# Performance work log

Hardware: AMD Instinct MI355X
Metric: run time of the kernel (lower is better)

The kernel has to match this reference:

```python
import jax, jax.numpy as jnp
import numpy as np

NUM_NODES = 100000
EMBED_DIM = 64
NUM_LAYERS = 3
NUM_EDGES = 1250000


def setup_inputs() -> dict:
    key = jax.random.key(0)
    k1, k2 = jax.random.split(key)
    edge_index = jax.random.randint(k1, (2, NUM_EDGES), 0, NUM_NODES, dtype=jnp.int64)
    emb_weight = jax.random.normal(k2, (NUM_NODES, EMBED_DIM), dtype=jnp.float32)
    alpha = jnp.full((NUM_LAYERS + 1,), 1.0 / (NUM_LAYERS + 1), dtype=jnp.float32)
    return {"edge_index": edge_index, "emb_weight": emb_weight, "alpha": alpha}


def reference(edge_index, emb_weight, alpha):
    # edge_index: [2, E] int; emb_weight: [N, d]; alpha: [L+1]
    row, col = edge_index[0], edge_index[1]  # source, target (flow source_to_target)
    N = emb_weight.shape[0]

    # gcn_norm without self-loops: deg over target index, symmetric normalization
    deg = jax.ops.segment_sum(jnp.ones_like(row, dtype=emb_weight.dtype), col, num_segments=N)
    dis = jnp.where(deg > 0, jax.lax.rsqrt(jnp.maximum(deg, 1.0)), 0.0)
    w = dis[row] * dis[col]  # [E]

    x = emb_weight
    out = x * alpha[0]
    for i in range(NUM_LAYERS):
        # gather-scale-scatter: out[col] += w * x[row]
        msg = x[row] * w[:, None]  # [E, d]
        x = jax.ops.segment_sum(msg, col, num_segments=N)
        out = out + x * alpha[i + 1]

    # edge_label_index defaults to edge_index -> dot-product ranking per edge
    return jnp.sum(out[row] * out[col], axis=-1)  # [E]
```

## Files before the change

### kernel.cpp

```cpp
#include <hip/hip_runtime.h>

#define EDIM 64
#define CHUNK 4096
#define BSH 9
#define BCOLS 512
#define CAP 8192
#define PAD 8
#define MAXPADB ((PAD - 1) * BCOLS)

__device__ __forceinline__ unsigned f2_to_bf2(float a, float b) {
    unsigned ua = __float_as_uint(a); ua += 0x7fffu + ((ua >> 16) & 1u);
    unsigned ub = __float_as_uint(b); ub += 0x7fffu + ((ub >> 16) & 1u);
    return (ua >> 16) | (ub & 0xffff0000u);
}
__device__ __forceinline__ float bf_lo(unsigned u) { return __uint_as_float(u << 16); }
__device__ __forceinline__ float bf_hi(unsigned u) { return __uint_as_float(u & 0xffff0000u); }

__global__ void k_binit(int* __restrict__ bcur, int nb) {
    int b = threadIdx.x;
    if (b < nb) bcur[b] = b * CAP;
}

__global__ __launch_bounds__(256) void k_binA(const int* __restrict__ row, const int* __restrict__ col,
                                              int* __restrict__ bcur, uint2* __restrict__ pairs,
                                              int E, int nb) {
    __shared__ uint2 buf[CHUNK];
    __shared__ int histL[256], baseL[256], curL[256], gbaseL[256];
    __shared__ int wsum[4];
    int tid = threadIdx.x;
    int c0 = blockIdx.x * CHUNK;
    int cend = min(CHUNK, E - c0);

    histL[tid] = 0;
    __syncthreads();

    int myr[CHUNK / 256], myc[CHUNK / 256];
    #pragma unroll
    for (int k = 0; k < CHUNK / 256; ++k) {
        int i = k * 256 + tid;
        if (i < cend) {
            int e = c0 + i;
            myr[k] = row[e]; myc[k] = col[e];
            atomicAdd(&histL[myc[k] >> BSH], 1);
        }
    }
    __syncthreads();

    int v = histL[tid];
    int lane = tid & 63, w = tid >> 6;
    int inc = v;
    #pragma unroll
    for (int d = 1; d < 64; d <<= 1) { int t = __shfl_up(inc, d, 64); if (lane >= d) inc += t; }
    if (lane == 63) wsum[w] = inc;
    __syncthreads();
    int woff = 0;
    for (int i = 0; i < w; ++i) woff += wsum[i];
    int excl = inc - v + woff;
    baseL[tid] = excl;
    curL[tid] = excl;
    if (tid < nb) gbaseL[tid] = atomicAdd(&bcur[tid], v);
    __syncthreads();

    #pragma unroll
    for (int k = 0; k < CHUNK / 256; ++k) {
        int i = k * 256 + tid;
        if (i < cend) {
            int b = myc[k] >> BSH;
            int e = c0 + i;
            int pos = atomicAdd(&curL[b], 1);
            buf[pos] = make_uint2((unsigned)myr[k] | ((unsigned)b << 24),
                                  ((unsigned)e << 9) | ((unsigned)myc[k] & (BCOLS - 1)));
        }
    }
    __syncthreads();

    for (int i = tid; i < cend; i += 256) {
        uint2 p = buf[i];
        int b = (int)(p.x >> 24);
        int dst = gbaseL[b] + (i - baseL[b]);
        pairs[dst] = make_uint2(p.x & 0x00FFFFFFu, p.y);
    }
}

__global__ void k_bscan(const int* __restrict__ bcur, int* __restrict__ bbase, int nb) {
    __shared__ int wsum[4];
    int tid = threadIdx.x;
    int v = (tid < nb) ? (bcur[tid] - tid * CAP) : 0;
    int lane = tid & 63, w = tid >> 6;
    int inc = v;
    #pragma unroll
    for (int d = 1; d < 64; d <<= 1) { int t = __shfl_up(inc, d, 64); if (lane >= d) inc += t; }
    if (lane == 63) wsum[w] = inc;
    __syncthreads();
    int woff = 0;
    for (int i = 0; i < w; ++i) woff += wsum[i];
    if (tid < nb) bbase[tid] = inc - v + woff;
}

__global__ __launch_bounds__(256) void k_binB(const uint2* __restrict__ pairs,
                                              const int* __restrict__ bcur, const int* __restrict__ bbase,
                                              int* __restrict__ offS, int* __restrict__ offE,
                                              float* __restrict__ dis, float* __restrict__ invd,
                                              int* __restrict__ rowp, int* __restrict__ eidx,
                                              int N, int E) {
    __shared__ int degL[BCOLS];
    __shared__ int curL[BCOLS];
    __shared__ int wsum[4];
    int tid = threadIdx.x;
    int b = blockIdx.x;
    int base_in = b * CAP;
    int cnt = bcur[b] - base_in;
    int col0 = b << BSH;
    int ncols = min(BCOLS, N - col0);
    int Pb = bbase[b] + b * MAXPADB;

    degL[tid] = 0; degL[tid + 256] = 0;
    __syncthreads();

    for (int i = tid; i < cnt; i += 256)
        atomicAdd(&degL[(int)(pairs[base_in + i].y & (BCOLS - 1))], 1);
    __syncthreads();

    int d0 = degL[2 * tid], d1 = degL[2 * tid + 1];
    int p0 = (d0 + PAD - 1) & ~(PAD - 1);
    int p1 = (d1 + PAD - 1) & ~(PAD - 1);
    int v = p0 + p1;
    int lane = tid & 63, w = tid >> 6;
    int inc = v;
    #pragma unroll
    for (int d = 1; d < 64; d <<= 1) { int t = __shfl_up(inc, d, 64); if (lane >= d) inc += t; }
    if (lane == 63) wsum[w] = inc;
    __syncthreads();
    int woff = 0;
    for (int i = 0; i < w; ++i) woff += wsum[i];
    int exclp = inc - v + woff + Pb;
    __syncthreads();
    int c0i = 2 * tid, c1i = 2 * tid + 1;
    if (c0i < ncols) {
        offS[col0 + c0i] = exclp;
        offE[col0 + c0i] = exclp + p0;
        dis [col0 + c0i] = (d0 > 0) ? rsqrtf((float)d0) : 0.0f;
        invd[col0 + c0i] = (d0 > 0) ? sqrtf((float)d0) : 0.0f;
        curL[c0i] = exclp;
        for (int k = d0; k < p0; ++k) { rowp[exclp + k] = N; eidx[exclp + k] = E; }
    }
    if (c1i < ncols) {
        int e1 = exclp + p0;
        offS[col0 + c1i] = e1;
        offE[col0 + c1i] = e1 + p1;
        dis [col0 + c1i] = (d1 > 0) ? rsqrtf((float)d1) : 0.0f;
        invd[col0 + c1i] = (d1 > 0) ? sqrtf((float)d1) : 0.0f;
        curL[c1i] = e1;
        for (int k = d1; k < p1; ++k) { rowp[e1 + k] = N; eidx[e1 + k] = E; }
    }
    __syncthreads();

    for (int i = tid; i < cnt; i += 256) {
        uint2 p = pairs[base_in + i];
        int pos = atomicAdd(&curL[(int)(p.y & (BCOLS - 1))], 1);
        rowp[pos] = (int)p.x;
        eidx[pos] = (int)(p.y >> 9);
    }
}

__global__ __launch_bounds__(256) void k_cvty(const float* __restrict__ emb,
                                              const float* __restrict__ dis,
                                              unsigned* __restrict__ y0,
                                              unsigned* __restrict__ y1,
                                              unsigned* __restrict__ y2,
                                              unsigned* __restrict__ o16, int N) {
    int i = blockIdx.x * blockDim.x + threadIdx.x;
    int n16 = N * 16;
    if (i < n16) {
        float d = dis[i >> 4];
        float4 v = ((const float4*)emb)[i];
        uint2 o; o.x = f2_to_bf2(d * v.x, d * v.y); o.y = f2_to_bf2(d * v.z, d * v.w);
        ((uint2*)y0)[i] = o;
    } else if (i < n16 + 16) {
        uint2 z = make_uint2(0u, 0u);
        ((uint2*)y0)[i] = z;
        ((uint2*)y1)[i] = z;
        ((uint2*)y2)[i] = z;
        ((uint2*)o16)[i] = z;
    }
}

__global__ __launch_bounds__(256) void k_prop(const int* __restrict__ offS, const int* __restrict__ offE,
                                              const int* __restrict__ rowp,
                                              const float* __restrict__ dis, const float* __restrict__ invd,
                                              const unsigned short* __restrict__ yin,
                                              unsigned short* __restrict__ yout,
                                              const float* __restrict__ emb,
                                              const unsigned short* __restrict__ y1,
                                              const unsigned short* __restrict__ y2,
                                              const float* __restrict__ alpha,
                                              unsigned short* __restrict__ out16,
                                              int N, int last) {
    int t = blockIdx.x * blockDim.x + threadIdx.x;
    int wid = t >> 3;
    if (wid >= N) return;
    int q = threadIdx.x & 7;
    int j0 = offS[wid];
    int j1 = offE[wid];
    float s0 = 0.f, s1 = 0.f, s2 = 0.f, s3 = 0.f, s4 = 0.f, s5 = 0.f, s6 = 0.f, s7 = 0.f;

    for (int j = j0; j < j1; j += 8) {
        int r0 = rowp[j],     r1 = rowp[j + 1], r2 = rowp[j + 2], r3 = rowp[j + 3];
        int r4 = rowp[j + 4], r5 = rowp[j + 5], r6 = rowp[j + 6], r7 = rowp[j + 7];
        uint4 v0 = *(const uint4*)(yin + ((size_t)r0 << 6) + (q << 3));
        uint4 v1 = *(const uint4*)(yin + ((size_t)r1 << 6) + (q << 3));
        uint4 v2 = *(const uint4*)(yin + ((size_t)r2 << 6) + (q << 3));
        uint4 v3 = *(const uint4*)(yin + ((size_t)r3 << 6) + (q << 3));
        uint4 v4 = *(const uint4*)(yin + ((size_t)r4 << 6) + (q << 3));
        uint4 v5 = *(const uint4*)(yin + ((size_t)r5 << 6) + (q << 3));
        uint4 v6 = *(const uint4*)(yin + ((size_t)r6 << 6) + (q << 3));
        uint4 v7 = *(const uint4*)(yin + ((size_t)r7 << 6) + (q << 3));
        s0 += bf_lo(v0.x) + bf_lo(v1.x) + bf_lo(v2.x) + bf_lo(v3.x)
            + bf_lo(v4.x) + bf_lo(v5.x) + bf_lo(v6.x) + bf_lo(v7.x);
        s1 += bf_hi(v0.x) + bf_hi(v1.x) + bf_hi(v2.x) + bf_hi(v3.x)
            + bf_hi(v4.x) + bf_hi(v5.x) + bf_hi(v6.x) + bf_hi(v7.x);
        s2 += bf_lo(v0.y) + bf_lo(v1.y) + bf_lo(v2.y) + bf_lo(v3.y)
            + bf_lo(v4.y) + bf_lo(v5.y) + bf_lo(v6.y) + bf_lo(v7.y);
        s3 += bf_hi(v0.y) + bf_hi(v1.y) + bf_hi(v2.y) + bf_hi(v3.y)
            + bf_hi(v4.y) + bf_hi(v5.y) + bf_hi(v6.y) + bf_hi(v7.y);
        s4 += bf_lo(v0.z) + bf_lo(v1.z) + bf_lo(v2.z) + bf_lo(v3.z)
            + bf_lo(v4.z) + bf_lo(v5.z) + bf_lo(v6.z) + bf_lo(v7.z);
        s5 += bf_hi(v0.z) + bf_hi(v1.z) + bf_hi(v2.z) + bf_hi(v3.z)
            + bf_hi(v4.z) + bf_hi(v5.z) + bf_hi(v6.z) + bf_hi(v7.z);
        s6 += bf_lo(v0.w) + bf_lo(v1.w) + bf_lo(v2.w) + bf_lo(v3.w)
            + bf_lo(v4.w) + bf_lo(v5.w) + bf_lo(v6.w) + bf_lo(v7.w);
        s7 += bf_hi(v0.w) + bf_hi(v1.w) + bf_hi(v2.w) + bf_hi(v3.w)
            + bf_hi(v4.w) + bf_hi(v5.w) + bf_hi(v6.w) + bf_hi(v7.w);
    }

    float d = dis[wid];
    size_t oi = ((size_t)wid << 6) + (q << 3);
    if (!last) {
        float sc = d * d;
        uint4 o;
        o.x = f2_to_bf2(sc * s0, sc * s1);
        o.y = f2_to_bf2(sc * s2, sc * s3);
        o.z = f2_to_bf2(sc * s4, sc * s5);
        o.w = f2_to_bf2(sc * s6, sc * s7);
        *(uint4*)(yout + oi) = o;
    } else {
        float iv = invd[wid];
        float a0 = alpha[0], a1 = alpha[1], a2 = alpha[2], a3 = alpha[3];
        float4 ea = *(const float4*)(emb + oi);
        float4 eb = *(const float4*)(emb + oi + 4);
        uint4 u1 = *(const uint4*)(y1 + oi);
        uint4 u2 = *(const uint4*)(y2 + oi);
        float o0 = a0 * ea.x + iv * (a1 * bf_lo(u1.x) + a2 * bf_lo(u2.x)) + a3 * d * s0;
        float o1 = a0 * ea.y + iv * (a1 * bf_hi(u1.x) + a2 * bf_hi(u2.x)) + a3 * d * s1;
        float o2 = a0 * ea.z + iv * (a1 * bf_lo(u1.y) + a2 * bf_lo(u2.y)) + a3 * d * s2;
        float o3 = a0 * ea.w + iv * (a1 * bf_hi(u1.y) + a2 * bf_hi(u2.y)) + a3 * d * s3;
        float o4 = a0 * eb.x + iv * (a1 * bf_lo(u1.z) + a2 * bf_lo(u2.z)) + a3 * d * s4;
        float o5 = a0 * eb.y + iv * (a1 * bf_hi(u1.z) + a2 * bf_hi(u2.z)) + a3 * d * s5;
        float o6 = a0 * eb.z + iv * (a1 * bf_lo(u1.w) + a2 * bf_lo(u2.w)) + a3 * d * s6;
        float o7 = a0 * eb.w + iv * (a1 * bf_hi(u1.w) + a2 * bf_hi(u2.w)) + a3 * d * s7;
        uint4 o;
        o.x = f2_to_bf2(o0, o1);
        o.y = f2_to_bf2(o2, o3);
        o.z = f2_to_bf2(o4, o5);
        o.w = f2_to_bf2(o6, o7);
        *(uint4*)(out16 + oi) = o;
    }
}

__global__ __launch_bounds__(256) void k_dotc(const int* __restrict__ offS, const int* __restrict__ offE,
                                              const int* __restrict__ rowp,
                                              const int* __restrict__ eidx,
                                              const unsigned short* __restrict__ out16,
                                              float* __restrict__ res, int N, int E) {
    int t = blockIdx.x * blockDim.x + threadIdx.x;
    int wid = t >> 3;
    if (wid >= N) return;
    int q = threadIdx.x & 7;
    int j0 = offS[wid];
    int j1 = offE[wid];

    uint4 bv = *(const uint4*)(out16 + ((size_t)wid << 6) + (q << 3));

    for (int j = j0; j < j1; j += 8) {
        int r0 = rowp[j],     r1 = rowp[j + 1], r2 = rowp[j + 2], r3 = rowp[j + 3];
        int r4 = rowp[j + 4], r5 = rowp[j + 5], r6 = rowp[j + 6], r7 = rowp[j + 7];
        uint4 a0 = *(const uint4*)(out16 + ((size_t)r0 << 6) + (q << 3));
        uint4 a1 = *(const uint4*)(out16 + ((size_t)r1 << 6) + (q << 3));
        uint4 a2 = *(const uint4*)(out16 + ((size_t)r2 << 6) + (q << 3));
        uint4 a3 = *(const uint4*)(out16 + ((size_t)r3 << 6) + (q << 3));
        uint4 a4 = *(const uint4*)(out16 + ((size_t)r4 << 6) + (q << 3));
        uint4 a5 = *(const uint4*)(out16 + ((size_t)r5 << 6) + (q << 3));
        uint4 a6 = *(const uint4*)(out16 + ((size_t)r6 << 6) + (q << 3));
        uint4 a7 = *(const uint4*)(out16 + ((size_t)r7 << 6) + (q << 3));
        #define DOT8(av) (bf_lo(av.x)*bf_lo(bv.x) + bf_hi(av.x)*bf_hi(bv.x) \
                        + bf_lo(av.y)*bf_lo(bv.y) + bf_hi(av.y)*bf_hi(bv.y) \
                        + bf_lo(av.z)*bf_lo(bv.z) + bf_hi(av.z)*bf_hi(bv.z) \
                        + bf_lo(av.w)*bf_lo(bv.w) + bf_hi(av.w)*bf_hi(bv.w))
        float t0 = DOT8(a0), t1 = DOT8(a1), t2 = DOT8(a2), t3 = DOT8(a3);
        float t4 = DOT8(a4), t5 = DOT8(a5), t6 = DOT8(a6), t7 = DOT8(a7);
        #undef DOT8
        t0 += __shfl_xor(t0, 1, 8); t1 += __shfl_xor(t1, 1, 8);
        t2 += __shfl_xor(t2, 1, 8); t3 += __shfl_xor(t3, 1, 8);
        t4 += __shfl_xor(t4, 1, 8); t5 += __shfl_xor(t5, 1, 8);
        t6 += __shfl_xor(t6, 1, 8); t7 += __shfl_xor(t7, 1, 8);
        t0 += __shfl_xor(t0, 2, 8); t1 += __shfl_xor(t1, 2, 8);
        t2 += __shfl_xor(t2, 2, 8); t3 += __shfl_xor(t3, 2, 8);
        t4 += __shfl_xor(t4, 2, 8); t5 += __shfl_xor(t5, 2, 8);
        t6 += __shfl_xor(t6, 2, 8); t7 += __shfl_xor(t7, 2, 8);
        t0 += __shfl_xor(t0, 4, 8); t1 += __shfl_xor(t1, 4, 8);
        t2 += __shfl_xor(t2, 4, 8); t3 += __shfl_xor(t3, 4, 8);
        t4 += __shfl_xor(t4, 4, 8); t5 += __shfl_xor(t5, 4, 8);
        t6 += __shfl_xor(t6, 4, 8); t7 += __shfl_xor(t7, 4, 8);
        if (q == 0) {
            int e0 = eidx[j],     e1 = eidx[j + 1], e2 = eidx[j + 2], e3 = eidx[j + 3];
            int e4 = eidx[j + 4], e5 = eidx[j + 5], e6 = eidx[j + 6], e7 = eidx[j + 7];
            if (e0 < E) res[e0] = t0;
            if (e1 < E) res[e1] = t1;
            if (e2 < E) res[e2] = t2;
            if (e3 < E) res[e3] = t3;
            if (e4 < E) res[e4] = t4;
            if (e5 < E) res[e5] = t5;
            if (e6 < E) res[e6] = t6;
            if (e7 < E) res[e7] = t7;
        }
    }
}

extern "C" void kernel_launch(void* const* d_in, const int* in_sizes, int n_in,
                              void* d_out, int out_size, void* d_ws, size_t ws_size,
                              hipStream_t stream) {
    const int*   edge  = (const int*)d_in[0];
    const float* emb   = (const float*)d_in[1];
    const float* alpha = (const float*)d_in[2];
    float*       res   = (float*)d_out;

    const int E = in_sizes[0] / 2;
    const int N = in_sizes[1] / EDIM;
    const int* row = edge;
    const int* col = edge + E;
    const int NB = (N + BCOLS - 1) >> BSH;
    const size_t EPAD = (size_t)E + (size_t)NB * MAXPADB + 64;

    size_t o = 0;
    int*   offS  = (int*)d_ws + o;   o += (size_t)N;
    int*   offE  = (int*)d_ws + o;   o += (size_t)N;
    float* dis   = (float*)d_ws + o; o += (size_t)N;
    float* invd  = (float*)d_ws + o; o += (size_t)N;
    int*   bcur  = (int*)d_ws + o;   o += 256;
    int*   bbase = (int*)d_ws + o;   o += 256;
    int*   rowp  = (int*)d_ws + o;   o += EPAD;
    int*   eidx  = (int*)d_ws + o;   o += EPAD;
    unsigned short* y0 = (unsigned short*)((int*)d_ws + o); o += (size_t)(N + 1) * 32;
    unsigned short* y1 = (unsigned short*)((int*)d_ws + o); o += (size_t)(N + 1) * 32;
    unsigned short* y2 = (unsigned short*)((int*)d_ws + o); o += (size_t)(N + 1) * 32;
    uint2* pairs = (uint2*)((int*)d_ws + o);
    unsigned short* out16 = (unsigned short*)pairs;
    (void)ws_size; (void)n_in;

    const int B = 256;

    k_binit<<<1, 256, 0, stream>>>(bcur, NB);
    k_binA <<<(E + CHUNK - 1) / CHUNK, B, 0, stream>>>(row, col, bcur, pairs, E, NB);
    k_bscan<<<1, 256, 0, stream>>>(bcur, bbase, NB);
    k_binB <<<NB, B, 0, stream>>>(pairs, bcur, bbase, offS, offE, dis, invd, rowp, eidx, N, E);

    k_cvty <<<(N * 16 + 16 + B - 1) / B, B, 0, stream>>>(emb, dis, (unsigned*)y0,
                                                         (unsigned*)y1, (unsigned*)y2,
                                                         (unsigned*)out16, N);

    k_prop<<<((size_t)N * 8 + B - 1) / B, B, 0, stream>>>(
        offS, offE, rowp, dis, invd, y0, y1, emb, y1, y2, alpha, out16, N, 0);
    k_prop<<<((size_t)N * 8 + B - 1) / B, B, 0, stream>>>(
        offS, offE, rowp, dis, invd, y1, y2, emb, y1, y2, alpha, out16, N, 0);
    k_prop<<<((size_t)N * 8 + B - 1) / B, B, 0, stream>>>(
        offS, offE, rowp, dis, invd, y2, (unsigned short*)0, emb, y1, y2, alpha, out16, N, 1);

    k_dotc<<<((size_t)N * 8 + B - 1) / B, B, 0, stream>>>(offS, offE, rowp, eidx, out16, res, N, E);
}
```

Measured before the change: 181.3 us.

## Fuse bucket scan and bf16 conversion into binB, prefetch row indices

Drops the separate bucket-scan kernel: every binB block now redoes the small prefix scan over bucket counts and keeps only its own base. The embedding pre-scale and bf16 conversion kernel is also folded into binB, using degree-normalisation values held in shared memory, which removes two launches and one reread of `dis`. The propagation and dot kernels now load the next group of row indices before the current feature loads are used, overlapping index latency with gathers. Result writes switch to nontemporal stores. The risks are redundant scan work in every block, extra rowp reads past the segment end (covered by padding), and zeroing the `out16` row (which aliases `pairs`) while other binB blocks may still be reading `pairs`.

```diff
diff --git a/kernel.cpp b/kernel.cpp
--- a/kernel.cpp
+++ b/kernel.cpp
@@ -82,45 +82,48 @@
     }
 }
 
-__global__ void k_bscan(const int* __restrict__ bcur, int* __restrict__ bbase, int nb) {
-    __shared__ int wsum[4];
-    int tid = threadIdx.x;
-    int v = (tid < nb) ? (bcur[tid] - tid * CAP) : 0;
-    int lane = tid & 63, w = tid >> 6;
-    int inc = v;
-    #pragma unroll
-    for (int d = 1; d < 64; d <<= 1) { int t = __shfl_up(inc, d, 64); if (lane >= d) inc += t; }
-    if (lane == 63) wsum[w] = inc;
-    __syncthreads();
-    int woff = 0;
-    for (int i = 0; i < w; ++i) woff += wsum[i];
-    if (tid < nb) bbase[tid] = inc - v + woff;
-}
-
 __global__ __launch_bounds__(256) void k_binB(const uint2* __restrict__ pairs,
-                                              const int* __restrict__ bcur, const int* __restrict__ bbase,
+                                              const int* __restrict__ bcur,
                                               int* __restrict__ offS, int* __restrict__ offE,
                                               float* __restrict__ dis, float* __restrict__ invd,
                                               int* __restrict__ rowp, int* __restrict__ eidx,
-                                              int N, int E) {
+                                              const float* __restrict__ emb,
+                                              unsigned* __restrict__ y0, unsigned* __restrict__ y1,
+                                              unsigned* __restrict__ y2, unsigned* __restrict__ o16,
+                                              int N, int E, int NB) {
     __shared__ int degL[BCOLS];
     __shared__ int curL[BCOLS];
+    __shared__ float disL[BCOLS];
     __shared__ int wsum[4];
+    __shared__ int bbaseS;
     int tid = threadIdx.x;
     int b = blockIdx.x;
     int base_in = b * CAP;
     int cnt = bcur[b] - base_in;
     int col0 = b << BSH;
     int ncols = min(BCOLS, N - col0);
-    int Pb = bbase[b] + b * MAXPADB;
 
     degL[tid] = 0; degL[tid + 256] = 0;
+
+    {
+        int v = (tid < NB) ? (bcur[tid] - tid * CAP) : 0;
+        int lane = tid & 63, w = tid >> 6;
+        int inc = v;
+        #pragma unroll
+        for (int d = 1; d < 64; d <<= 1) { int t = __shfl_up(inc, d, 64); if (lane >= d) inc += t; }
+        if (lane == 63) wsum[w] = inc;
+        __syncthreads();
+        int woff = 0;
+        for (int i = 0; i < w; ++i) woff += wsum[i];
+        if (tid == b) bbaseS = inc - v + woff;
+    }
     __syncthreads();
 
     for (int i = tid; i < cnt; i += 256)
         atomicAdd(&degL[(int)(pairs[base_in + i].y & (BCOLS - 1))], 1);
     __syncthreads();
 
+    int Pb = bbaseS + b * MAXPADB;
     int d0 = degL[2 * tid], d1 = degL[2 * tid + 1];
     int p0 = (d0 + PAD - 1) & ~(PAD - 1);
     int p1 = (d1 + PAD - 1) & ~(PAD - 1);
@@ -137,19 +140,23 @@
     __syncthreads();
     int c0i = 2 * tid, c1i = 2 * tid + 1;
     if (c0i < ncols) {
+        float dv = (d0 > 0) ? rsqrtf((float)d0) : 0.0f;
         offS[col0 + c0i] = exclp;
         offE[col0 + c0i] = exclp + p0;
-        dis [col0 + c0i] = (d0 > 0) ? rsqrtf((float)d0) : 0.0f;
+        dis [col0 + c0i] = dv;
         invd[col0 + c0i] = (d0 > 0) ? sqrtf((float)d0) : 0.0f;
+        disL[c0i] = dv;
         curL[c0i] = exclp;
         for (int k = d0; k < p0; ++k) { rowp[exclp + k] = N; eidx[exclp + k] = E; }
     }
     if (c1i < ncols) {
+        float dv = (d1 > 0) ? rsqrtf((float)d1) : 0.0f;
         int e1 = exclp + p0;
         offS[col0 + c1i] = e1;
         offE[col0 + c1i] = e1 + p1;
-        dis [col0 + c1i] = (d1 > 0) ? rsqrtf((float)d1) : 0.0f;
+        dis [col0 + c1i] = dv;
         invd[col0 + c1i] = (d1 > 0) ? sqrtf((float)d1) : 0.0f;
+        disL[c1i] = dv;
         curL[c1i] = e1;
         for (int k = d1; k < p1; ++k) { rowp[e1 + k] = N; eidx[e1 + k] = E; }
     }
@@ -161,27 +168,23 @@
         rowp[pos] = (int)p.x;
         eidx[pos] = (int)(p.y >> 9);
     }
-}
-
-__global__ __launch_bounds__(256) void k_cvty(const float* __restrict__ emb,
-                                              const float* __restrict__ dis,
-                                              unsigned* __restrict__ y0,
-                                              unsigned* __restrict__ y1,
-                                              unsigned* __restrict__ y2,
-                                              unsigned* __restrict__ o16, int N) {
-    int i = blockIdx.x * blockDim.x + threadIdx.x;
-    int n16 = N * 16;
-    if (i < n16) {
-        float d = dis[i >> 4];
-        float4 v = ((const float4*)emb)[i];
-        uint2 o; o.x = f2_to_bf2(d * v.x, d * v.y); o.y = f2_to_bf2(d * v.z, d * v.w);
-        ((uint2*)y0)[i] = o;
-    } else if (i < n16 + 16) {
+
+    for (int i = tid; i < ncols * 16; i += 256) {
+        int r = i >> 4, u = i & 15;
+        float dv = disL[r];
+        float4 vv = ((const float4*)(emb + ((size_t)(col0 + r) << 6)))[u];
+        uint2 ov;
+        ov.x = f2_to_bf2(dv * vv.x, dv * vv.y);
+        ov.y = f2_to_bf2(dv * vv.z, dv * vv.w);
+        ((uint2*)y0)[((size_t)(col0 + r) << 4) + u] = ov;
+    }
+    if (b == 0 && tid < 16) {
         uint2 z = make_uint2(0u, 0u);
-        ((uint2*)y0)[i] = z;
-        ((uint2*)y1)[i] = z;
-        ((uint2*)y2)[i] = z;
-        ((uint2*)o16)[i] = z;
+        size_t di = ((size_t)N << 4) + tid;
+        ((uint2*)y0)[di] = z;
+        ((uint2*)y1)[di] = z;
+        ((uint2*)y2)[di] = z;
+        ((uint2*)o16)[di] = z;
     }
 }
 
@@ -204,17 +207,21 @@
     int j1 = offE[wid];
     float s0 = 0.f, s1 = 0.f, s2 = 0.f, s3 = 0.f, s4 = 0.f, s5 = 0.f, s6 = 0.f, s7 = 0.f;
 
+    int rc0 = rowp[j0],     rc1 = rowp[j0 + 1], rc2 = rowp[j0 + 2], rc3 = rowp[j0 + 3];
+    int rc4 = rowp[j0 + 4], rc5 = rowp[j0 + 5], rc6 = rowp[j0 + 6], rc7 = rowp[j0 + 7];
+
     for (int j = j0; j < j1; j += 8) {
-        int r0 = rowp[j],     r1 = rowp[j + 1], r2 = rowp[j + 2], r3 = rowp[j + 3];
-        int r4 = rowp[j + 4], r5 = rowp[j + 5], r6 = rowp[j + 6], r7 = rowp[j + 7];
-        uint4 v0 = *(const uint4*)(yin + ((size_t)r0 << 6) + (q << 3));
-        uint4 v1 = *(const uint4*)(yin + ((size_t)r1 << 6) + (q << 3));
-        uint4 v2 = *(const uint4*)(yin + ((size_t)r2 << 6) + (q << 3));
-        uint4 v3 = *(const uint4*)(yin + ((size_t)r3 << 6) + (q << 3));
-        uint4 v4 = *(const uint4*)(yin + ((size_t)r4 << 6) + (q << 3));
-        uint4 v5 = *(const uint4*)(yin + ((size_t)r5 << 6) + (q << 3));
-        uint4 v6 = *(const uint4*)(yin + ((size_t)r6 << 6) + (q << 3));
-        uint4 v7 = *(const uint4*)(yin + ((size_t)r7 << 6) + (q << 3));
+        uint4 v0 = *(const uint4*)(yin + ((size_t)rc0 << 6) + (q << 3));
+        uint4 v1 = *(const uint4*)(yin + ((size_t)rc1 << 6) + (q << 3));
+        uint4 v2 = *(const uint4*)(yin + ((size_t)rc2 << 6) + (q << 3));
+        uint4 v3 = *(const uint4*)(yin + ((size_t)rc3 << 6) + (q << 3));
+        uint4 v4 = *(const uint4*)(yin + ((size_t)rc4 << 6) + (q << 3));
+        uint4 v5 = *(const uint4*)(yin + ((size_t)rc5 << 6) + (q << 3));
+        uint4 v6 = *(const uint4*)(yin + ((size_t)rc6 << 6) + (q << 3));
+        uint4 v7 = *(const uint4*)(yin + ((size_t)rc7 << 6) + (q << 3));
+        int nj = j + 8;
+        rc0 = rowp[nj];     rc1 = rowp[nj + 1]; rc2 = rowp[nj + 2]; rc3 = rowp[nj + 3];
+        rc4 = rowp[nj + 4]; rc5 = rowp[nj + 5]; rc6 = rowp[nj + 6]; rc7 = rowp[nj + 7];
         s0 += bf_lo(v0.x) + bf_lo(v1.x) + bf_lo(v2.x) + bf_lo(v3.x)
             + bf_lo(v4.x) + bf_lo(v5.x) + bf_lo(v6.x) + bf_lo(v7.x);
         s1 += bf_hi(v0.x) + bf_hi(v1.x) + bf_hi(v2.x) + bf_hi(v3.x)
@@ -281,17 +288,21 @@
 
     uint4 bv = *(const uint4*)(out16 + ((size_t)wid << 6) + (q << 3));
 
+    int rc0 = rowp[j0],     rc1 = rowp[j0 + 1], rc2 = rowp[j0 + 2], rc3 = rowp[j0 + 3];
+    int rc4 = rowp[j0 + 4], rc5 = rowp[j0 + 5], rc6 = rowp[j0 + 6], rc7 = rowp[j0 + 7];
+
     for (int j = j0; j < j1; j += 8) {
-        int r0 = rowp[j],     r1 = rowp[j + 1], r2 = rowp[j + 2], r3 = rowp[j + 3];
-        int r4 = rowp[j + 4], r5 = rowp[j + 5], r6 = rowp[j + 6], r7 = rowp[j + 7];
-        uint4 a0 = *(const uint4*)(out16 + ((size_t)r0 << 6) + (q << 3));
-        uint4 a1 = *(const uint4*)(out16 + ((size_t)r1 << 6) + (q << 3));
-        uint4 a2 = *(const uint4*)(out16 + ((size_t)r2 << 6) + (q << 3));
-        uint4 a3 = *(const uint4*)(out16 + ((size_t)r3 << 6) + (q << 3));
-        uint4 a4 = *(const uint4*)(out16 + ((size_t)r4 << 6) + (q << 3));
-        uint4 a5 = *(const uint4*)(out16 + ((size_t)r5 << 6) + (q << 3));
-        uint4 a6 = *(const uint4*)(out16 + ((size_t)r6 << 6) + (q << 3));
-        uint4 a7 = *(const uint4*)(out16 + ((size_t)r7 << 6) + (q << 3));
+        uint4 a0 = *(const uint4*)(out16 + ((size_t)rc0 << 6) + (q << 3));
+        uint4 a1 = *(const uint4*)(out16 + ((size_t)rc1 << 6) + (q << 3));
+        uint4 a2 = *(const uint4*)(out16 + ((size_t)rc2 << 6) + (q << 3));
+        uint4 a3 = *(const uint4*)(out16 + ((size_t)rc3 << 6) + (q << 3));
+        uint4 a4 = *(const uint4*)(out16 + ((size_t)rc4 << 6) + (q << 3));
+        uint4 a5 = *(const uint4*)(out16 + ((size_t)rc5 << 6) + (q << 3));
+        uint4 a6 = *(const uint4*)(out16 + ((size_t)rc6 << 6) + (q << 3));
+        uint4 a7 = *(const uint4*)(out16 + ((size_t)rc7 << 6) + (q << 3));
+        int nj = j + 8;
+        rc0 = rowp[nj];     rc1 = rowp[nj + 1]; rc2 = rowp[nj + 2]; rc3 = rowp[nj + 3];
+        rc4 = rowp[nj + 4]; rc5 = rowp[nj + 5]; rc6 = rowp[nj + 6]; rc7 = rowp[nj + 7];
         #define DOT8(av) (bf_lo(av.x)*bf_lo(bv.x) + bf_hi(av.x)*bf_hi(bv.x) \
                         + bf_lo(av.y)*bf_lo(bv.y) + bf_hi(av.y)*bf_hi(bv.y) \
                         + bf_lo(av.z)*bf_lo(bv.z) + bf_hi(av.z)*bf_hi(bv.z) \
@@ -314,14 +325,14 @@
         if (q == 0) {
             int e0 = eidx[j],     e1 = eidx[j + 1], e2 = eidx[j + 2], e3 = eidx[j + 3];
             int e4 = eidx[j + 4], e5 = eidx[j + 5], e6 = eidx[j + 6], e7 = eidx[j + 7];
-            if (e0 < E) res[e0] = t0;
-            if (e1 < E) res[e1] = t1;
-            if (e2 < E) res[e2] = t2;
-            if (e3 < E) res[e3] = t3;
-            if (e4 < E) res[e4] = t4;
-            if (e5 < E) res[e5] = t5;
-            if (e6 < E) res[e6] = t6;
-            if (e7 < E) res[e7] = t7;
+            if (e0 < E) __builtin_nontemporal_store(t0, &res[e0]);
+            if (e1 < E) __builtin_nontemporal_store(t1, &res[e1]);
+            if (e2 < E) __builtin_nontemporal_store(t2, &res[e2]);
+            if (e3 < E) __builtin_nontemporal_store(t3, &res[e3]);
+            if (e4 < E) __builtin_nontemporal_store(t4, &res[e4]);
+            if (e5 < E) __builtin_nontemporal_store(t5, &res[e5]);
+            if (e6 < E) __builtin_nontemporal_store(t6, &res[e6]);
+            if (e7 < E) __builtin_nontemporal_store(t7, &res[e7]);
         }
     }
 }
@@ -347,7 +358,6 @@
     float* dis   = (float*)d_ws + o; o += (size_t)N;
     float* invd  = (float*)d_ws + o; o += (size_t)N;
     int*   bcur  = (int*)d_ws + o;   o += 256;
-    int*   bbase = (int*)d_ws + o;   o += 256;
     int*   rowp  = (int*)d_ws + o;   o += EPAD;
     int*   eidx  = (int*)d_ws + o;   o += EPAD;
     unsigned short* y0 = (unsigned short*)((int*)d_ws + o); o += (size_t)(N + 1) * 32;
@@ -361,12 +371,9 @@
 
     k_binit<<<1, 256, 0, stream>>>(bcur, NB);
     k_binA <<<(E + CHUNK - 1) / CHUNK, B, 0, stream>>>(row, col, bcur, pairs, E, NB);
-    k_bscan<<<1, 256, 0, stream>>>(bcur, bbase, NB);
-    k_binB <<<NB, B, 0, stream>>>(pairs, bcur, bbase, offS, offE, dis, invd, rowp, eidx, N, E);
-
-    k_cvty <<<(N * 16 + 16 + B - 1) / B, B, 0, stream>>>(emb, dis, (unsigned*)y0,
-                                                         (unsigned*)y1, (unsigned*)y2,
-                                                         (unsigned*)out16, N);
+    k_binB <<<NB, B, 0, stream>>>(pairs, bcur, offS, offE, dis, invd, rowp, eidx,
+                                  emb, (unsigned*)y0, (unsigned*)y1, (unsigned*)y2,
+                                  (unsigned*)out16, N, E, NB);
 
     k_prop<<<((size_t)N * 8 + B - 1) / B, B, 0, stream>>>(
         offS, offE, rowp, dis, invd, y0, y1, emb, y1, y2, alpha, out16, N, 0);
```

Result: no change. 180.8 us (-0.2%).
